# Kernel optimization log

Measured on AMD Instinct MI355X. Metric: run time of the kernel, lower is better.

The kernel has to match this reference:

```python
import jax, jax.numpy as jnp
import numpy as np

N = 50000   # nodes
E = 400000  # edges
IN_DIM, H1, H2, OUT_DIM = 512, 256, 62, 128


def _param(key, shape, scale=0.05):
    return jax.random.normal(key, shape, dtype=jnp.float32) * scale


def setup_inputs() -> dict:
    key = jax.random.key(0)
    ks = jax.random.split(key, 24)
    x = jax.random.normal(ks[0], (N, IN_DIM), dtype=jnp.float32)
    edge_index_neg = jax.random.randint(ks[1], (2, E), 0, N, dtype=jnp.int64)
    d = {
        "x": x, "edge_index_neg": edge_index_neg,
        # nn.Linear params (W stored as [in, out])
        "W1": _param(ks[2], (IN_DIM, H1)), "b1": _param(ks[3], (H1,)),
        "W2": _param(ks[4], (H1, H2)),    "b2": _param(ks[5], (H2,)),
        "W3": _param(ks[6], (H2, OUT_DIM)), "b3": _param(ks[7], (OUT_DIM,)),
        # GCNConv params: lin weight (no bias) + post-aggregation bias
        "Wg1": _param(ks[8], (H1, H1)),   "bg1": _param(ks[9], (H1,)),
        "Wg2": _param(ks[10], (H2, H2)),  "bg2": _param(ks[11], (H2,)),
        "Wg3": _param(ks[12], (OUT_DIM, OUT_DIM)), "bg3": _param(ks[13], (OUT_DIM,)),
        "Wg4": _param(ks[14], (OUT_DIM, OUT_DIM)), "bg4": _param(ks[15], (OUT_DIM,)),
        "Wg5": _param(ks[16], (OUT_DIM, OUT_DIM)), "bg5": _param(ks[17], (OUT_DIM,)),
        "Wg6": _param(ks[18], (OUT_DIM, OUT_DIM)), "bg6": _param(ks[19], (OUT_DIM,)),
    }
    return d


def _build_norm(edge_index):
    # PyG GCNConv: add self-loops, symmetric normalization D^-1/2 A D^-1/2
    loop = jnp.arange(N, dtype=edge_index.dtype)
    src = jnp.concatenate([edge_index[0], loop])
    dst = jnp.concatenate([edge_index[1], loop])
    deg = jax.ops.segment_sum(jnp.ones_like(dst, dtype=jnp.float32), dst, num_segments=N)
    dinv = jnp.where(deg > 0, jax.lax.rsqrt(jnp.maximum(deg, 1.0)), 0.0)
    norm = dinv[src] * dinv[dst]  # [E+N]
    return src, dst, norm


def _gcn(x, W, b, src, dst, norm):
    h = x @ W                                   # [N, F]
    msg = h[src] * norm[:, None]                # gather + edge scale
    out = jax.ops.segment_sum(msg, dst, num_segments=N)  # scatter-add
    return out + b


def reference(x, edge_index_neg, W1, b1, W2, b2, W3, b3,
              Wg1, bg1, Wg2, bg2, Wg3, bg3, Wg4, bg4, Wg5, bg5, Wg6, bg6):
    src, dst, norm = _build_norm(edge_index_neg)
    relu = jax.nn.relu
    x1l = x @ W1 + b1
    x1 = x1l + relu(_gcn(x1l, Wg1, bg1, src, dst, norm))
    x2l = x1 @ W2 + b2
    x2 = x2l + relu(_gcn(x2l, Wg2, bg2, src, dst, norm))
    x3l = x2 @ W3 + b3
    x3 = x3l + 0.5 * relu(_gcn(x3l, Wg3, bg3, src, dst, norm))
    x4 = x3 + 0.5 * relu(_gcn(x4_in := x3, Wg4, bg4, src, dst, norm))
    x5 = x4 + 0.25 * relu(_gcn(x4, Wg5, bg5, src, dst, norm))
    x6 = x5 + 0.25 * _gcn(x5, Wg6, bg6, src, dst, norm)
    return x6
```

## Files before the change

### kernel.cpp

```cpp
#include <hip/hip_runtime.h>

#define NN 50000
#define NE 400000
#define NBLK 196

using short8 = __attribute__((ext_vector_type(8))) short;
using f32x4  = __attribute__((ext_vector_type(4))) float;
using u16x2  = __attribute__((ext_vector_type(2))) unsigned short;
using u16x4  = __attribute__((ext_vector_type(4))) unsigned short;

__device__ __forceinline__ unsigned short f2b(float f) {
    union { float f; unsigned int u; } x; x.f = f;
    unsigned int u = x.u;
    u += 0x7fffu + ((u >> 16) & 1u);
    return (unsigned short)(u >> 16);
}
__device__ __forceinline__ float b2f(unsigned short u) {
    union { unsigned int u; float f; } x; x.u = ((unsigned int)u) << 16;
    return x.f;
}

#define SWZ(b, row) ((b) ^ (((row) & 7) << 4))

__global__ __launch_bounds__(256) void zero2_k(int* a, int* b) {
    int i = blockIdx.x * 256 + threadIdx.x;
    if (i < NN) { a[i] = 0; b[i] = 0; }
}
__global__ __launch_bounds__(256) void count_k(const int* __restrict__ dst, int* __restrict__ indeg) {
    int e = blockIdx.x * 256 + threadIdx.x;
    if (e < NE) atomicAdd(&indeg[dst[e]], 1);
}
__global__ __launch_bounds__(256) void scan1_k(const int* __restrict__ indeg, int* __restrict__ tmp,
                                               int* __restrict__ bsum) {
    __shared__ int s[256];
    int t = threadIdx.x, i = blockIdx.x * 256 + t;
    int v = (i < NN) ? indeg[i] : 0;
    s[t] = v; __syncthreads();
    for (int off = 1; off < 256; off <<= 1) {
        int x = (t >= off) ? s[t - off] : 0;
        __syncthreads();
        s[t] += x;
        __syncthreads();
    }
    if (i < NN) tmp[i] = s[t];
    if (t == 255) bsum[blockIdx.x] = s[255];
}
__global__ __launch_bounds__(256) void scan2_k(const int* __restrict__ bsum, int* __restrict__ boff) {
    __shared__ int s[256];
    int t = threadIdx.x;
    int v = (t < NBLK) ? bsum[t] : 0;
    s[t] = v; __syncthreads();
    for (int off = 1; off < 256; off <<= 1) {
        int x = (t >= off) ? s[t - off] : 0;
        __syncthreads();
        s[t] += x;
        __syncthreads();
    }
    if (t < NBLK) boff[t] = s[t] - v;
}
__global__ __launch_bounds__(256) void scan3_k(const int* __restrict__ tmp, const int* __restrict__ indeg,
                                               const int* __restrict__ boff, int* __restrict__ rowptr,
                                               float* __restrict__ dinv) {
    int i = blockIdx.x * 256 + threadIdx.x;
    if (i < NN) {
        rowptr[i] = tmp[i] - indeg[i] + boff[i >> 8];
        dinv[i] = rsqrtf((float)(1 + indeg[i]));
    }
    if (i == 0) rowptr[NN] = NE;
}
__global__ __launch_bounds__(256) void fill_k(const int* __restrict__ src, const int* __restrict__ dst,
                                              const float* __restrict__ dinv, const int* __restrict__ rowptr,
                                              int* __restrict__ cursor, int2* __restrict__ ebn) {
    int e = blockIdx.x * 256 + threadIdx.x;
    if (e >= NE) return;
    int s = src[e], d = dst[e];
    int pos = atomicAdd(&cursor[d], 1);
    ebn[rowptr[d] + pos] = make_int2(s, __float_as_int(dinv[s] * dinv[d]));
}

struct WSegs {
    const float* W[9];
    unsigned short* Wt[9];
    int K[9], N[9], Kp[9];
    int c0[10];
};
__global__ __launch_bounds__(256) void wcast_all_k(WSegs s) {
    int blk = blockIdx.x;
    #pragma unroll
    for (int g = 0; g < 9; g++) {
        if (blk >= s.c0[g] && blk < s.c0[g + 1]) {
            int idx = (blk - s.c0[g]) * 256 + threadIdx.x;
            int Kp = s.Kp[g];
            int n = idx / Kp, k = idx % Kp;
            float v = (n < s.N[g] && k < s.K[g]) ? s.W[g][(size_t)k * s.N[g] + n] : 0.0f;
            s.Wt[g][idx] = f2b(v);
        }
    }
}

template<bool AF32, int BM, int BN>
__global__ __launch_bounds__(256) void gemm_mfma_k(
    const void* __restrict__ Araw, const unsigned short* __restrict__ Bt,
    const float* __restrict__ bias, unsigned short* __restrict__ C,
    int M, int lda, int Kp, int N, int ldc) {
    constexpr int MR = BM / 32;
    constexpr int NF = BN / 32;
    constexpr int nA = BM / 32;
    constexpr int nB = BN / 32;
    constexpr int BUFB = (BM + BN) * 128;
    __shared__ __align__(16) char lds[2 * BUFB];

    int tid = threadIdx.x;
    int lane = tid & 63, wave = tid >> 6;
    int wr = wave >> 1, wc = wave & 1;
    int lr = lane & 15, lk = lane >> 4;
    int r0 = blockIdx.x * BM, c0 = blockIdx.y * BN;

    f32x4 acc[MR][NF];
    #pragma unroll
    for (int m = 0; m < MR; m++)
        #pragma unroll
        for (int n = 0; n < NF; n++)
            acc[m][n] = (f32x4){0.f, 0.f, 0.f, 0.f};

    float4 fa0[nA], fa1[nA];
    short8 ra[nA], rb[nB];

    auto LOAD = [&](int k0) {
        #pragma unroll
        for (int c = 0; c < nA; c++) {
            int o = tid + c * 256, row = o >> 3, oct = o & 7;
            int gr = r0 + row;
            if constexpr (AF32) {
                if (gr < M) {
                    const float* p = (const float*)Araw + (size_t)gr * lda + k0 + oct * 8;
                    fa0[c] = *(const float4*)p;
                    fa1[c] = *(const float4*)(p + 4);
                } else {
                    fa0[c] = make_float4(0, 0, 0, 0);
                    fa1[c] = make_float4(0, 0, 0, 0);
                }
            } else {
                short8 z = {0, 0, 0, 0, 0, 0, 0, 0};
                ra[c] = (gr < M)
                    ? *(const short8*)((const unsigned short*)Araw + (size_t)gr * lda + k0 + oct * 8)
                    : z;
            }
        }
        #pragma unroll
        for (int c = 0; c < nB; c++) {
            int o = tid + c * 256, row = o >> 3, oct = o & 7;
            rb[c] = *(const short8*)(Bt + (size_t)(c0 + row) * Kp + k0 + oct * 8);
        }
    };
    auto STORE = [&](char* AsB, char* BsB) {
        #pragma unroll
        for (int c = 0; c < nA; c++) {
            int o = tid + c * 256, row = o >> 3, oct = o & 7;
            short8 v;
            if constexpr (AF32) {
                v[0] = (short)f2b(fa0[c].x); v[1] = (short)f2b(fa0[c].y);
                v[2] = (short)f2b(fa0[c].z); v[3] = (short)f2b(fa0[c].w);
                v[4] = (short)f2b(fa1[c].x); v[5] = (short)f2b(fa1[c].y);
                v[6] = (short)f2b(fa1[c].z); v[7] = (short)f2b(fa1[c].w);
            } else {
                v = ra[c];
            }
            *(short8*)(AsB + SWZ(row * 128 + oct * 16, row)) = v;
        }
        #pragma unroll
        for (int c = 0; c < nB; c++) {
            int o = tid + c * 256, row = o >> 3, oct = o & 7;
            *(short8*)(BsB + SWZ(row * 128 + oct * 16, row)) = rb[c];
        }
    };

    int nt = Kp >> 6;
    LOAD(0);
    STORE(lds, lds + BM * 128);
    __syncthreads();
    for (int t = 0; t < nt; t++) {
        char* cur = lds + (t & 1) * BUFB;
        char* alt = lds + ((t + 1) & 1) * BUFB;
        if (t + 1 < nt) LOAD((t + 1) << 6);
        char* AsB = cur;
        char* BsB = cur + BM * 128;
        #pragma unroll
        for (int kk = 0; kk < 2; kk++) {
            int kb = kk * 64 + lk * 16;
            short8 a[MR], b[NF];
            #pragma unroll
            for (int m = 0; m < MR; m++) {
                int row = wr * (BM / 2) + m * 16 + lr;
                a[m] = *(short8*)(AsB + SWZ(row * 128 + kb, row));
            }
            #pragma unroll
            for (int n = 0; n < NF; n++) {
                int row = wc * (BN / 2) + n * 16 + lr;
                b[n] = *(short8*)(BsB + SWZ(row * 128 + kb, row));
            }
            #pragma unroll
            for (int m = 0; m < MR; m++)
                #pragma unroll
                for (int n = 0; n < NF; n++)
                    acc[m][n] = __builtin_amdgcn_mfma_f32_16x16x32_bf16(a[m], b[n], acc[m][n], 0, 0, 0);
        }
        if (t + 1 < nt) STORE(alt, alt + BM * 128);
        __syncthreads();
    }

    constexpr int LDC = BN + 8;
    unsigned short* ldsC = (unsigned short*)lds;
    #pragma unroll
    for (int n = 0; n < NF; n++) {
        int cc = wc * (BN / 2) + n * 16 + lr;
        int gc = c0 + cc;
        float bv = (bias != nullptr && gc < N) ? bias[gc] : 0.0f;
        bool ok = gc < N;
        #pragma unroll
        for (int m = 0; m < MR; m++)
            #pragma unroll
            for (int j = 0; j < 4; j++) {
                int row = wr * (BM / 2) + m * 16 + lk * 4 + j;
                float v = ok ? acc[m][n][j] + bv : 0.0f;
                ldsC[row * LDC + cc] = f2b(v);
            }
    }
    __syncthreads();
    constexpr int CH = (BM * BN) / 2048;
    #pragma unroll
    for (int c = 0; c < CH; c++) {
        int o = tid + c * 256;
        int row = o / (BN / 8), col = (o % (BN / 8)) * 8;
        int gr = r0 + row;
        if (gr < M)
            *(short8*)(C + (size_t)gr * ldc + c0 + col) = *(short8*)(ldsC + row * LDC + col);
    }
}

template<int VEC> struct BV;
template<> struct BV<1> { using T = unsigned short; };
template<> struct BV<2> { using T = u16x2; };
template<> struct BV<4> { using T = u16x4; };

template<int VEC, bool OUTF32>
__global__ __launch_bounds__(256) void gather_k(
    const unsigned short* __restrict__ h, const unsigned short* __restrict__ base,
    const float* __restrict__ dinv, const float* __restrict__ bias,
    const int2* __restrict__ ebn, const int* __restrict__ rowptr,
    void* __restrict__ outraw, float alpha, int dorelu, int F) {
    const int ld = 64 * VEC;
    int w = (blockIdx.x * 256 + threadIdx.x) >> 6;
    int lane = threadIdx.x & 63;
    if (w >= NN) return;
    using LT = typename BV<VEC>::T;

    float acc[VEC];
    float dn = dinv[w];
    {
        LT t = *(const LT*)(h + (size_t)w * ld + lane * VEC);
        const unsigned short* tu = (const unsigned short*)&t;
        #pragma unroll
        for (int v = 0; v < VEC; v++) acc[v] = b2f(tu[v]) * dn * dn;
    }
    int e = rowptr[w], end = rowptr[w + 1];
    for (; e + 8 <= end; e += 8) {
        int2 q[8];
        #pragma unroll
        for (int i = 0; i < 8; i++) q[i] = ebn[e + i];
        LT t[8];
        #pragma unroll
        for (int i = 0; i < 8; i++) t[i] = *(const LT*)(h + (size_t)q[i].x * ld + lane * VEC);
        #pragma unroll
        for (int i = 0; i < 8; i++) {
            float nr = __int_as_float(q[i].y);
            const unsigned short* u = (const unsigned short*)&t[i];
            #pragma unroll
            for (int v = 0; v < VEC; v++) acc[v] += b2f(u[v]) * nr;
        }
    }
    for (; e + 2 <= end; e += 2) {
        int2 q0 = ebn[e], q1 = ebn[e + 1];
        LT t0 = *(const LT*)(h + (size_t)q0.x * ld + lane * VEC);
        LT t1 = *(const LT*)(h + (size_t)q1.x * ld + lane * VEC);
        float n0 = __int_as_float(q0.y), n1 = __int_as_float(q1.y);
        const unsigned short* u0 = (const unsigned short*)&t0;
        const unsigned short* u1 = (const unsigned short*)&t1;
        #pragma unroll
        for (int v = 0; v < VEC; v++) acc[v] += b2f(u0[v]) * n0 + b2f(u1[v]) * n1;
    }
    if (e < end) {
        int2 q0 = ebn[e];
        LT t0 = *(const LT*)(h + (size_t)q0.x * ld + lane * VEC);
        float n0 = __int_as_float(q0.y);
        const unsigned short* u0 = (const unsigned short*)&t0;
        #pragma unroll
        for (int v = 0; v < VEC; v++) acc[v] += b2f(u0[v]) * n0;
    }
    LT bt = *(const LT*)(base + (size_t)w * ld + lane * VEC);
    const unsigned short* bu = (const unsigned short*)&bt;
    #pragma unroll
    for (int v = 0; v < VEC; v++) {
        int f = lane * VEC + v;
        float a = acc[v] + ((f < F) ? bias[f] : 0.0f);
        if (dorelu) a = fmaxf(a, 0.0f);
        float res = (f < F) ? b2f(bu[v]) + alpha * a : 0.0f;
        if (OUTF32) ((float*)outraw)[(size_t)w * ld + f] = res;
        else        ((unsigned short*)outraw)[(size_t)w * ld + f] = f2b(res);
    }
}

extern "C" void kernel_launch(void* const* d_in, const int* in_sizes, int n_in,
                              void* d_out, int out_size, void* d_ws, size_t ws_size,
                              hipStream_t stream) {
    const float* x   = (const float*)d_in[0];
    const int*   ei  = (const int*)d_in[1];
    const float* W1  = (const float*)d_in[2];  const float* b1  = (const float*)d_in[3];
    const float* W2  = (const float*)d_in[4];  const float* b2  = (const float*)d_in[5];
    const float* W3  = (const float*)d_in[6];  const float* b3  = (const float*)d_in[7];
    const float* Wg1 = (const float*)d_in[8];  const float* bg1 = (const float*)d_in[9];
    const float* Wg2 = (const float*)d_in[10]; const float* bg2 = (const float*)d_in[11];
    const float* Wg3 = (const float*)d_in[12]; const float* bg3 = (const float*)d_in[13];
    const float* Wg4 = (const float*)d_in[14]; const float* bg4 = (const float*)d_in[15];
    const float* Wg5 = (const float*)d_in[16]; const float* bg5 = (const float*)d_in[17];
    const float* Wg6 = (const float*)d_in[18]; const float* bg6 = (const float*)d_in[19];
    const int* srcv = ei;
    const int* dstv = ei + NE;

    float* dinv = (float*)d_ws;
    unsigned short* hA = (unsigned short*)(dinv + 51200);
    unsigned short* hB = hA + (size_t)NN * 256;
    unsigned short* hC = hB + (size_t)NN * 256;
    unsigned short* W1t  = hC + (size_t)NN * 256;
    unsigned short* Wg1t = W1t  + 256 * 512;
    unsigned short* W2t  = Wg1t + 256 * 256;
    unsigned short* Wg2t = W2t  + 64 * 256;
    unsigned short* W3t  = Wg2t + 64 * 64;
    unsigned short* Wg3t = W3t  + 128 * 64;
    unsigned short* Wg4t = Wg3t + 128 * 128;
    unsigned short* Wg5t = Wg4t + 128 * 128;
    unsigned short* Wg6t = Wg5t + 128 * 128;
    int* indeg  = (int*)(Wg6t + 128 * 128);
    int* cursor = indeg + 51200;
    int* tmp    = cursor + 51200;
    int* rowptr = tmp + 51200;
    int* bsum   = rowptr + 51264;
    int* boff   = bsum + 256;
    int2* ebn   = (int2*)(boff + 256);

    zero2_k<<<NBLK, 256, 0, stream>>>(indeg, cursor);
    count_k<<<(NE + 255) / 256, 256, 0, stream>>>(dstv, indeg);
    scan1_k<<<NBLK, 256, 0, stream>>>(indeg, tmp, bsum);
    scan2_k<<<1, 256, 0, stream>>>(bsum, boff);
    scan3_k<<<NBLK, 256, 0, stream>>>(tmp, indeg, boff, rowptr, dinv);
    fill_k<<<(NE + 255) / 256, 256, 0, stream>>>(srcv, dstv, dinv, rowptr, cursor, ebn);

    {
        WSegs s;
        const float* Ws[9] = {W1, Wg1, W2, Wg2, W3, Wg3, Wg4, Wg5, Wg6};
        unsigned short* Wts[9] = {W1t, Wg1t, W2t, Wg2t, W3t, Wg3t, Wg4t, Wg5t, Wg6t};
        int Ks[9]  = {512, 256, 256, 62, 62, 128, 128, 128, 128};
        int Ns[9]  = {256, 256, 62, 62, 128, 128, 128, 128, 128};
        int Kps[9] = {512, 256, 256, 64, 64, 128, 128, 128, 128};
        int Nps[9] = {256, 256, 64, 64, 128, 128, 128, 128, 128};
        int c = 0;
        for (int g = 0; g < 9; g++) {
            s.W[g] = Ws[g]; s.Wt[g] = Wts[g];
            s.K[g] = Ks[g]; s.N[g] = Ns[g]; s.Kp[g] = Kps[g];
            s.c0[g] = c;
            c += (Kps[g] * Nps[g]) / 256;
        }
        s.c0[9] = c;
        wcast_all_k<<<c, 256, 0, stream>>>(s);
    }

    const int GX = (NN + 63) / 64;
    const int GG = (NN * 64 + 255) / 256;

    gemm_mfma_k<true, 64, 128><<<dim3(GX, 2), 256, 0, stream>>>(x, W1t, b1, hA, NN, 512, 512, 256, 256);
    gemm_mfma_k<false, 64, 128><<<dim3(GX, 2), 256, 0, stream>>>(hA, Wg1t, nullptr, hB, NN, 256, 256, 256, 256);
    gather_k<4, false><<<GG, 256, 0, stream>>>(hB, hA, dinv, bg1, ebn, rowptr, hC, 1.0f, 1, 256);
    gemm_mfma_k<false, 64, 64><<<dim3(GX, 1), 256, 0, stream>>>(hC, W2t, b2, hA, NN, 256, 256, 62, 64);
    gemm_mfma_k<false, 64, 64><<<dim3(GX, 1), 256, 0, stream>>>(hA, Wg2t, nullptr, hB, NN, 64, 64, 62, 64);
    gather_k<1, false><<<GG, 256, 0, stream>>>(hB, hA, dinv, bg2, ebn, rowptr, hC, 1.0f, 1, 62);
    gemm_mfma_k<false, 64, 128><<<dim3(GX, 1), 256, 0, stream>>>(hC, W3t, b3, hA, NN, 64, 64, 128, 128);
    gemm_mfma_k<false, 64, 128><<<dim3(GX, 1), 256, 0, stream>>>(hA, Wg3t, nullptr, hB, NN, 128, 128, 128, 128);
    gather_k<2, false><<<GG, 256, 0, stream>>>(hB, hA, dinv, bg3, ebn, rowptr, hC, 0.5f, 1, 128);
    gemm_mfma_k<false, 64, 128><<<dim3(GX, 1), 256, 0, stream>>>(hC, Wg4t, nullptr, hA, NN, 128, 128, 128, 128);
    gather_k<2, false><<<GG, 256, 0, stream>>>(hA, hC, dinv, bg4, ebn, rowptr, hB, 0.5f, 1, 128);
    gemm_mfma_k<false, 64, 128><<<dim3(GX, 1), 256, 0, stream>>>(hB, Wg5t, nullptr, hA, NN, 128, 128, 128, 128);
    gather_k<2, false><<<GG, 256, 0, stream>>>(hA, hB, dinv, bg5, ebn, rowptr, hC, 0.25f, 1, 128);
    gemm_mfma_k<false, 64, 128><<<dim3(GX, 1), 256, 0, stream>>>(hC, Wg6t, nullptr, hA, NN, 128, 128, 128, 128);
    gather_k<2, true><<<GG, 256, 0, stream>>>(hA, hC, dinv, bg6, ebn, rowptr, d_out, 0.25f, 0, 128);
}
```

Measured before the change: 383.1 us.

## Use direct global-to-LDS loads in GEMM and pre-cast x to bf16

Replaces the register-staged global load plus LDS store in the MFMA GEMM with global_load_lds 16-byte direct copies, moving the XOR swizzle onto the global source address and clamping out-of-range rows instead of zero-filling. Because this path cannot convert fp32 to bf16 on the fly, a separate xcast kernel converts x to a bf16 buffer first. This removes register pressure and VGPR round-trips in the GEMM main loop. In exchange it adds an extra full pass that reads x and writes a 51 MB bf16 copy. Synchronization relies on __syncthreads covering the async LDS writes, which may need explicit vmcnt waits.

After: 392.7 us. 2.5% more time.

```diff
diff --git a/kernel.cpp b/kernel.cpp
--- a/kernel.cpp
+++ b/kernel.cpp
@@ -21,6 +21,12 @@
 }
 
 #define SWZ(b, row) ((b) ^ (((row) & 7) << 4))
+
+__device__ __forceinline__ void gload16(const void* g, void* l) {
+    __builtin_amdgcn_global_load_lds(
+        (const __attribute__((address_space(1))) void*)g,
+        (__attribute__((address_space(3))) void*)l, 16, 0, 0);
+}
 
 __global__ __launch_bounds__(256) void zero2_k(int* a, int* b) {
     int i = blockIdx.x * 256 + threadIdx.x;
@@ -78,6 +84,20 @@
     ebn[rowptr[d] + pos] = make_int2(s, __float_as_int(dinv[s] * dinv[d]));
 }
 
+__global__ __launch_bounds__(256) void xcast_k(const float* __restrict__ x, unsigned short* __restrict__ xb) {
+    long i = (long)blockIdx.x * 256 + threadIdx.x;
+    const long total = (long)NN * 512 / 8;
+    if (i >= total) return;
+    float4 f0 = *(const float4*)(x + i * 8);
+    float4 f1 = *(const float4*)(x + i * 8 + 4);
+    short8 v;
+    v[0] = (short)f2b(f0.x); v[1] = (short)f2b(f0.y);
+    v[2] = (short)f2b(f0.z); v[3] = (short)f2b(f0.w);
+    v[4] = (short)f2b(f1.x); v[5] = (short)f2b(f1.y);
+    v[6] = (short)f2b(f1.z); v[7] = (short)f2b(f1.w);
+    *(short8*)(xb + i * 8) = v;
+}
+
 struct WSegs {
     const float* W[9];
     unsigned short* Wt[9];
@@ -98,9 +118,9 @@
     }
 }
 
-template<bool AF32, int BM, int BN>
+template<int BM, int BN>
 __global__ __launch_bounds__(256) void gemm_mfma_k(
-    const void* __restrict__ Araw, const unsigned short* __restrict__ Bt,
+    const unsigned short* __restrict__ A, const unsigned short* __restrict__ Bt,
     const float* __restrict__ bias, unsigned short* __restrict__ C,
     int M, int lda, int Kp, int N, int ldc) {
     constexpr int MR = BM / 32;
@@ -123,66 +143,32 @@
         for (int n = 0; n < NF; n++)
             acc[m][n] = (f32x4){0.f, 0.f, 0.f, 0.f};
 
-    float4 fa0[nA], fa1[nA];
-    short8 ra[nA], rb[nB];
-
-    auto LOAD = [&](int k0) {
+    auto ISSUE = [&](int k0, char* buf) {
+        char* AsB = buf;
+        char* BsB = buf + BM * 128;
         #pragma unroll
         for (int c = 0; c < nA; c++) {
-            int o = tid + c * 256, row = o >> 3, oct = o & 7;
-            int gr = r0 + row;
-            if constexpr (AF32) {
-                if (gr < M) {
-                    const float* p = (const float*)Araw + (size_t)gr * lda + k0 + oct * 8;
-                    fa0[c] = *(const float4*)p;
-                    fa1[c] = *(const float4*)(p + 4);
-                } else {
-                    fa0[c] = make_float4(0, 0, 0, 0);
-                    fa1[c] = make_float4(0, 0, 0, 0);
-                }
-            } else {
-                short8 z = {0, 0, 0, 0, 0, 0, 0, 0};
-                ra[c] = (gr < M)
-                    ? *(const short8*)((const unsigned short*)Araw + (size_t)gr * lda + k0 + oct * 8)
-                    : z;
-            }
+            int o = tid + c * 256;
+            int row = o >> 3;
+            int octg = (o & 7) ^ (row & 7);
+            int gr = min(r0 + row, M - 1);
+            gload16(A + (size_t)gr * lda + k0 + octg * 8, AsB + o * 16);
         }
         #pragma unroll
         for (int c = 0; c < nB; c++) {
-            int o = tid + c * 256, row = o >> 3, oct = o & 7;
-            rb[c] = *(const short8*)(Bt + (size_t)(c0 + row) * Kp + k0 + oct * 8);
+            int o = tid + c * 256;
+            int row = o >> 3;
+            int octg = (o & 7) ^ (row & 7);
+            gload16(Bt + (size_t)(c0 + row) * Kp + k0 + octg * 8, BsB + o * 16);
         }
     };
-    auto STORE = [&](char* AsB, char* BsB) {
-        #pragma unroll
-        for (int c = 0; c < nA; c++) {
-            int o = tid + c * 256, row = o >> 3, oct = o & 7;
-            short8 v;
-            if constexpr (AF32) {
-                v[0] = (short)f2b(fa0[c].x); v[1] = (short)f2b(fa0[c].y);
-                v[2] = (short)f2b(fa0[c].z); v[3] = (short)f2b(fa0[c].w);
-                v[4] = (short)f2b(fa1[c].x); v[5] = (short)f2b(fa1[c].y);
-                v[6] = (short)f2b(fa1[c].z); v[7] = (short)f2b(fa1[c].w);
-            } else {
-                v = ra[c];
-            }
-            *(short8*)(AsB + SWZ(row * 128 + oct * 16, row)) = v;
-        }
-        #pragma unroll
-        for (int c = 0; c < nB; c++) {
-            int o = tid + c * 256, row = o >> 3, oct = o & 7;
-            *(short8*)(BsB + SWZ(row * 128 + oct * 16, row)) = rb[c];
-        }
-    };
 
     int nt = Kp >> 6;
-    LOAD(0);
-    STORE(lds, lds + BM * 128);
+    ISSUE(0, lds);
     __syncthreads();
     for (int t = 0; t < nt; t++) {
         char* cur = lds + (t & 1) * BUFB;
-        char* alt = lds + ((t + 1) & 1) * BUFB;
-        if (t + 1 < nt) LOAD((t + 1) << 6);
+        if (t + 1 < nt) ISSUE((t + 1) << 6, lds + ((t + 1) & 1) * BUFB);
         char* AsB = cur;
         char* BsB = cur + BM * 128;
         #pragma unroll
@@ -205,7 +191,6 @@
                 for (int n = 0; n < NF; n++)
                     acc[m][n] = __builtin_amdgcn_mfma_f32_16x16x32_bf16(a[m], b[n], acc[m][n], 0, 0, 0);
         }
-        if (t + 1 < nt) STORE(alt, alt + BM * 128);
         __syncthreads();
     }
 
@@ -328,7 +313,8 @@
     const int* dstv = ei + NE;
 
     float* dinv = (float*)d_ws;
-    unsigned short* hA = (unsigned short*)(dinv + 51200);
+    unsigned short* xb = (unsigned short*)(dinv + 51200);
+    unsigned short* hA = xb + (size_t)NN * 512;
     unsigned short* hB = hA + (size_t)NN * 256;
     unsigned short* hC = hB + (size_t)NN * 256;
     unsigned short* W1t  = hC + (size_t)NN * 256;
@@ -355,6 +341,8 @@
     scan3_k<<<NBLK, 256, 0, stream>>>(tmp, indeg, boff, rowptr, dinv);
     fill_k<<<(NE + 255) / 256, 256, 0, stream>>>(srcv, dstv, dinv, rowptr, cursor, ebn);
 
+    xcast_k<<<(int)(((long)NN * 512 / 8 + 255) / 256), 256, 0, stream>>>(x, xb);
+
     {
         WSegs s;
         const float* Ws[9] = {W1, Wg1, W2, Wg2, W3, Wg3, Wg4, Wg5, Wg6};
@@ -377,19 +365,19 @@
     const int GX = (NN + 63) / 64;
     const int GG = (NN * 64 + 255) / 256;
 
-    gemm_mfma_k<true, 64, 128><<<dim3(GX, 2), 256, 0, stream>>>(x, W1t, b1, hA, NN, 512, 512, 256, 256);
-    gemm_mfma_k<false, 64, 128><<<dim3(GX, 2), 256, 0, stream>>>(hA, Wg1t, nullptr, hB, NN, 256, 256, 256, 256);
+    gemm_mfma_k<64, 128><<<dim3(GX, 2), 256, 0, stream>>>(xb, W1t, b1, hA, NN, 512, 512, 256, 256);
+    gemm_mfma_k<64, 128><<<dim3(GX, 2), 256, 0, stream>>>(hA, Wg1t, nullptr, hB, NN, 256, 256, 256, 256);
     gather_k<4, false><<<GG, 256, 0, stream>>>(hB, hA, dinv, bg1, ebn, rowptr, hC, 1.0f, 1, 256);
-    gemm_mfma_k<false, 64, 64><<<dim3(GX, 1), 256, 0, stream>>>(hC, W2t, b2, hA, NN, 256, 256, 62, 64);
-    gemm_mfma_k<false, 64, 64><<<dim3(GX, 1), 256, 0, stream>>>(hA, Wg2t, nullptr, hB, NN, 64, 64, 62, 64);
+    gemm_mfma_k<64, 64><<<dim3(GX, 1), 256, 0, stream>>>(hC, W2t, b2, hA, NN, 256, 256, 62, 64);
+    gemm_mfma_k<64, 64><<<dim3(GX, 1), 256, 0, stream>>>(hA, Wg2t, nullptr, hB, NN, 64, 64, 62, 64);
     gather_k<1, false><<<GG, 256, 0, stream>>>(hB, hA, dinv, bg2, ebn, rowptr, hC, 1.0f, 1, 62);
-    gemm_mfma_k<false, 64, 128><<<dim3(GX, 1), 256, 0, stream>>>(hC, W3t, b3, hA, NN, 64, 64, 128, 128);
-    gemm_mfma_k<false, 64, 128><<<dim3(GX, 1), 256, 0, stream>>>(hA, Wg3t, nullptr, hB, NN, 128, 128, 128, 128);
+    gemm_mfma_k<64, 128><<<dim3(GX, 1), 256, 0, stream>>>(hC, W3t, b3, hA, NN, 64, 64, 128, 128);
+    gemm_mfma_k<64, 128><<<dim3(GX, 1), 256, 0, stream>>>(hA, Wg3t, nullptr, hB, NN, 128, 128, 128, 128);
     gather_k<2, false><<<GG, 256, 0, stream>>>(hB, hA, dinv, bg3, ebn, rowptr, hC, 0.5f, 1, 128);
-    gemm_mfma_k<false, 64, 128><<<dim3(GX, 1), 256, 0, stream>>>(hC, Wg4t, nullptr, hA, NN, 128, 128, 128, 128);
+    gemm_mfma_k<64, 128><<<dim3(GX, 1), 256, 0, stream>>>(hC, Wg4t, nullptr, hA, NN, 128, 128, 128, 128);
     gather_k<2, false><<<GG, 256, 0, stream>>>(hA, hC, dinv, bg4, ebn, rowptr, hB, 0.5f, 1, 128);
-    gemm_mfma_k<false, 64, 128><<<dim3(GX, 1), 256, 0, stream>>>(hB, Wg5t, nullptr, hA, NN, 128, 128, 128, 128);
+    gemm_mfma_k<64, 128><<<dim3(GX, 1), 256, 0, stream>>>(hB, Wg5t, nullptr, hA, NN, 128, 128, 128, 128);
     gather_k<2, false><<<GG, 256, 0, stream>>>(hA, hB, dinv, bg5, ebn, rowptr, hC, 0.25f, 1, 128);
-    gemm_mfma_k<false, 64, 128><<<dim3(GX, 1), 256, 0, stream>>>(hC, Wg6t, nullptr, hA, NN, 128, 128, 128, 128);
+    gemm_mfma_k<64, 128><<<dim3(GX, 1), 256, 0, stream>>>(hC, Wg6t, nullptr, hA, NN, 128, 128, 128, 128);
     gather_k<2, true><<<GG, 256, 0, stream>>>(hA, hC, dinv, bg6, ebn, rowptr, d_out, 0.25f, 0, 128);
 }
```
